# Performance work log

Measured on AMD Instinct MI355X. Metric: run time of the kernel, lower is better.

The kernel has to match this reference:

```python
import jax, jax.numpy as jnp
import numpy as np

N_NODES = 100_000
N_EDGES = 1_600_000
HIDDEN = 32


def setup_inputs() -> dict:
    key = jax.random.key(0)
    ks = jax.random.split(key, 8)
    pos = jax.random.normal(ks[0], (N_NODES, 3), dtype=jnp.float32)
    edge_index = jax.random.randint(ks[1], (2, N_EDGES), 0, N_NODES, dtype=jnp.int64)
    batch = jnp.zeros((N_NODES,), dtype=jnp.int64)
    # layer 1 MLP: Linear(3+3 -> 32) -> ReLU -> Linear(32 -> 32)
    W1 = jax.random.normal(ks[2], (6, HIDDEN), dtype=jnp.float32) * (1.0 / np.sqrt(6))
    b1 = jnp.zeros((HIDDEN,), dtype=jnp.float32)
    W2 = jax.random.normal(ks[3], (HIDDEN, HIDDEN), dtype=jnp.float32) * (1.0 / np.sqrt(HIDDEN))
    b2 = jnp.zeros((HIDDEN,), dtype=jnp.float32)
    # layer 2 MLP: Linear(32+3 -> 32) -> ReLU -> Linear(32 -> 32)
    W3 = jax.random.normal(ks[4], (HIDDEN + 3, HIDDEN), dtype=jnp.float32) * (1.0 / np.sqrt(HIDDEN + 3))
    b3 = jnp.zeros((HIDDEN,), dtype=jnp.float32)
    W4 = jax.random.normal(ks[5], (HIDDEN, HIDDEN), dtype=jnp.float32) * (1.0 / np.sqrt(HIDDEN))
    b4 = jnp.zeros((HIDDEN,), dtype=jnp.float32)
    return {"pos": pos, "edge_index": edge_index, "batch": batch,
            "W1": W1, "b1": b1, "W2": W2, "b2": b2,
            "W3": W3, "b3": b3, "W4": W4, "b4": b4}


def _pointnet_layer(h, rel, src, dst, n_nodes, Wa, ba, Wb, bb):
    # per-edge: concat(h_j, pos_j - pos_i) -> Linear -> ReLU -> Linear, then max-scatter into i
    e = jnp.concatenate([h[src], rel], axis=-1)             # [E, in+3]
    m = jax.nn.relu(e @ Wa + ba) @ Wb + bb                  # [E, out]
    agg = jax.ops.segment_max(m, dst, num_segments=n_nodes)  # [N, out], -inf for isolated nodes
    return jnp.where(jnp.isfinite(agg), agg, 0.0)


def reference(pos, edge_index, batch, W1, b1, W2, b2, W3, b3, W4, b4):
    src = edge_index[0]  # j (source)
    dst = edge_index[1]  # i (target, aggregation index)
    n_nodes = pos.shape[0]
    rel = pos[src] - pos[dst]  # [E, 3]
    h = jax.nn.relu(_pointnet_layer(pos, rel, src, dst, n_nodes, W1, b1, W2, b2))
    h = jax.nn.relu(_pointnet_layer(h, rel, src, dst, n_nodes, W3, b3, W4, b4))
    return h
```

## Files before the change

kernel.cpp:

```cpp
#include <hip/hip_runtime.h>
#include <hip/hip_bf16.h>
#include <stdint.h>


#define BS 256
#define EBS 512
#define K1_EDGES 4096
#define P2_CAP 3072

typedef float v2f __attribute__((ext_vector_type(2)));
typedef __attribute__((ext_vector_type(8))) short bf16x8;
typedef __attribute__((ext_vector_type(16))) float f32x16;
typedef __bf16 bf16v2 __attribute__((ext_vector_type(2)));

__device__ __forceinline__ unsigned ordenc(float f) {
    unsigned u = __float_as_uint(f);
    return (u & 0x80000000u) ? ~u : (u | 0x80000000u);
}
__device__ __forceinline__ float orddec(unsigned o) {
    unsigned u = (o & 0x80000000u) ? (o ^ 0x80000000u) : ~o;
    return __uint_as_float(u);
}
#define ORD_NEG_INF 0x007FFFFFu

__device__ __forceinline__ unsigned cvt2(float x, float y) {
    v2f v = {x, y};
    bf16v2 b = __builtin_convertvector(v, bf16v2);
    return __builtin_bit_cast(unsigned, b);
}
__device__ __forceinline__ float bflo(unsigned u) { return __uint_as_float(u << 16); }
__device__ __forceinline__ float bfhi(unsigned u) { return __uint_as_float(u & 0xFFFF0000u); }

__global__ __launch_bounds__(BS) void setup_kernel(
    const int* __restrict__ ei, int E, int NRP, int* __restrict__ blockHist,
    const float* __restrict__ pos, const float* __restrict__ Wa, const float* __restrict__ ba,
    unsigned* __restrict__ Ubf, float* __restrict__ V, int N, unsigned* __restrict__ aggA,
    unsigned* __restrict__ aggB, int n32, int NB1, int NBn) {
    __shared__ int hist[1024];
    const int tid = threadIdx.x;
    const int b = blockIdx.x;
    if (b < NB1) {
        for (int r = tid; r < 1024; r += BS) hist[r] = 0;
        __syncthreads();
        const int base = b * K1_EDGES;
        const int M = min(K1_EDGES, E - base);
        for (int i = tid; i < M; i += BS) atomicAdd(&hist[ei[E + base + i] >> 7], 1);
        __syncthreads();
        for (int r = tid; r < NRP; r += BS) blockHist[b * NRP + r] = hist[r];
    } else if (b < NB1 + NBn) {
        const int n = (b - NB1) * BS + tid;
        if (n >= N) return;
        const float p[3] = {pos[3 * n], pos[3 * n + 1], pos[3 * n + 2]};
        v2f u[16], v[16];
#pragma unroll
        for (int g = 0; g < 16; ++g) {
            u[g] = *reinterpret_cast<const v2f*>(&ba[g * 2]);
            v2f z = {0.0f, 0.0f};
            v[g] = z;
        }
#pragma unroll
        for (int i = 0; i < 3; ++i) {
            const v2f f = {p[i], p[i]};
#pragma unroll
            for (int g = 0; g < 16; ++g) {
                const v2f wA = *reinterpret_cast<const v2f*>(&Wa[i * 32 + g * 2]);
                const v2f wB = *reinterpret_cast<const v2f*>(&Wa[(i + 3) * 32 + g * 2]);
                u[g] = __builtin_elementwise_fma(f, wA + wB, u[g]);
                v[g] = __builtin_elementwise_fma(f, wB, v[g]);
            }
        }
        uint4* Up = reinterpret_cast<uint4*>(Ubf + (size_t)n * 16);
        float4* Vp = reinterpret_cast<float4*>(V + (size_t)n * 32);
#pragma unroll
        for (int q = 0; q < 4; ++q) {
            uint4 o;
            o.x = cvt2(u[4 * q + 0].x, u[4 * q + 0].y);
            o.y = cvt2(u[4 * q + 1].x, u[4 * q + 1].y);
            o.z = cvt2(u[4 * q + 2].x, u[4 * q + 2].y);
            o.w = cvt2(u[4 * q + 3].x, u[4 * q + 3].y);
            Up[q] = o;
        }
#pragma unroll
        for (int q = 0; q < 8; ++q)
            Vp[q] = make_float4(v[2 * q].x, v[2 * q].y, v[2 * q + 1].x, v[2 * q + 1].y);
    } else {
        const int i = (b - NB1 - NBn) * BS + tid;
        if (i < n32) {
            aggA[i] = ORD_NEG_INF;
            aggB[i] = ORD_NEG_INF;
        }
    }
}

__global__ __launch_bounds__(BS) void finalize_kernel(unsigned* __restrict__ buf, int n) {
    int i = blockIdx.x * BS + threadIdx.x;
    if (i < n) {
        float v = orddec(buf[i]);
        reinterpret_cast<float*>(buf)[i] = fmaxf(v, 0.0f);
    }
}

__global__ __launch_bounds__(512) void off_scan_kernel(const int* __restrict__ blockHist,
                                                       int NB1, int NRP,
                                                       int* __restrict__ off,
                                                       int* __restrict__ total) {
    const int r = (blockIdx.x * 512 + threadIdx.x) >> 6;
    const int lane = threadIdx.x & 63;
    if (r >= NRP) return;
    int carry = 0;
    const int chunks = (NB1 + 63) / 64;
    for (int c = 0; c < chunks; ++c) {
        const int b = c * 64 + lane;
        const int v = (b < NB1) ? blockHist[b * NRP + r] : 0;
        int x = v;
#pragma unroll
        for (int d = 1; d < 64; d <<= 1) {
            int y = __shfl_up(x, d, 64);
            if (lane >= d) x += y;
        }
        if (b < NB1) off[b * NRP + r] = carry + (x - v);
        carry += __shfl(x, 63, 64);
    }
    if (lane == 0) total[r] = carry;
}

__global__ __launch_bounds__(1024) void range_scan_kernel(const int* __restrict__ total,
                                                          int NRP, int* __restrict__ rangeBase) {
    __shared__ int s[1024];
    const int t = threadIdx.x;
    const int v = (t < NRP) ? total[t] : 0;
    s[t] = v;
    __syncthreads();
    for (int off = 1; off < 1024; off <<= 1) {
        int add = (t >= off) ? s[t - off] : 0;
        __syncthreads();
        s[t] += add;
        __syncthreads();
    }
    if (t < NRP) rangeBase[t] = s[t] - v;
}

__global__ __launch_bounds__(BS) void bucket_scatter_kernel(
    const int* __restrict__ ei, int E, int NRP, const int* __restrict__ off,
    const int* __restrict__ rangeBase, int2* __restrict__ sedgeB) {
    __shared__ int2 stage[K1_EDGES];
    __shared__ unsigned short inv[K1_EDGES];
    __shared__ int hist[1024], start[1024], cursor[1024];
    __shared__ int ts[BS];
    const int tid = threadIdx.x;
    for (int r = tid; r < 1024; r += BS) hist[r] = 0;
    __syncthreads();
    const int base = blockIdx.x * K1_EDGES;
    const int M = min(K1_EDGES, E - base);
    for (int i = tid; i < M; i += BS) {
        const int2 p = make_int2(ei[base + i], ei[E + base + i]);
        stage[i] = p;
        atomicAdd(&hist[p.y >> 7], 1);
    }
    __syncthreads();
    {
        const int i0 = tid * 4;
        const int l0 = hist[i0], l1 = hist[i0 + 1], l2 = hist[i0 + 2], l3 = hist[i0 + 3];
        const int tsum = l0 + l1 + l2 + l3;
        ts[tid] = tsum;
        __syncthreads();
        for (int off2 = 1; off2 < BS; off2 <<= 1) {
            int add = (tid >= off2) ? ts[tid - off2] : 0;
            __syncthreads();
            ts[tid] += add;
            __syncthreads();
        }
        const int texcl = ts[tid] - tsum;
        start[i0] = texcl;
        start[i0 + 1] = texcl + l0;
        start[i0 + 2] = texcl + l0 + l1;
        start[i0 + 3] = texcl + l0 + l1 + l2;
        cursor[i0] = start[i0];
        cursor[i0 + 1] = start[i0 + 1];
        cursor[i0 + 2] = start[i0 + 2];
        cursor[i0 + 3] = start[i0 + 3];
    }
    __syncthreads();
    for (int i = tid; i < M; i += BS) {
        const int pos = atomicAdd(&cursor[stage[i].y >> 7], 1);
        inv[pos] = (unsigned short)i;
    }
    __syncthreads();
    const int* offb = off + blockIdx.x * NRP;
    for (int j = tid; j < M; j += BS) {
        const int2 p = stage[inv[j]];
        const int r = p.y >> 7;
        sedgeB[rangeBase[r] + offb[r] + (j - start[r])] = p;
    }
}

__global__ __launch_bounds__(BS) void bucket_sort_kernel(
    const int2* __restrict__ sedgeB, const int* __restrict__ rangeBase,
    const int* __restrict__ total, int N, int2* __restrict__ sedge, int* __restrict__ row_ptr,
    int* __restrict__ cnt) {
    __shared__ int2 stage[P2_CAP];
    __shared__ unsigned short inv[P2_CAP];
    __shared__ int hist[128], start[128], cursor[128];
    const int r = blockIdx.x;
    const int tid = threadIdx.x;
    const int base = rangeBase[r];
    const int M = total[r];
    const bool fast = (M <= P2_CAP);
    if (tid < 128) hist[tid] = 0;
    __syncthreads();
    if (fast) {
        for (int i = tid; i < M; i += BS) {
            const int2 p = sedgeB[base + i];
            stage[i] = p;
            atomicAdd(&hist[p.y & 127], 1);
        }
    } else {
        if (tid < 128) {
            int c = 0;
            for (int i = 0; i < M; ++i) c += ((sedgeB[base + i].y & 127) == tid);
            hist[tid] = c;
        }
    }
    __syncthreads();
    if (tid < 128) start[tid] = hist[tid];
    __syncthreads();
    for (int off2 = 1; off2 < 128; off2 <<= 1) {
        int add = 0;
        if (tid < 128 && tid >= off2) add = start[tid - off2];
        __syncthreads();
        if (tid < 128) start[tid] += add;
        __syncthreads();
    }
    if (tid < 128) {
        const int excl = start[tid] - hist[tid];
        start[tid] = excl;
        cursor[tid] = excl;
        const int node = r * 128 + tid;
        if (node < N) {
            row_ptr[node] = base + excl;
            cnt[node] = hist[tid];
        }
    }
    __syncthreads();
    if (fast) {
        for (int i = tid; i < M; i += BS) {
            const int pos = atomicAdd(&cursor[stage[i].y & 127], 1);
            inv[pos] = (unsigned short)i;
        }
        __syncthreads();
        for (int j = tid; j < M; j += BS) sedge[base + j] = stage[inv[j]];
    } else {
        if (tid < 128) {
            int c = base + start[tid];
            for (int i = 0; i < M; ++i) {
                const int2 p = sedgeB[base + i];
                if ((p.y & 127) == tid) sedge[c++] = p;
            }
        }
    }
}

__global__ __launch_bounds__(BS) void prep2_kernel(const float* __restrict__ pos,
                                                   const unsigned* __restrict__ aggA,
                                                   const float* __restrict__ Wa,
                                                   const float* __restrict__ ba,
                                                   unsigned* __restrict__ Ubf,
                                                   float* __restrict__ V, int N) {
    int n = blockIdx.x * BS + threadIdx.x;
    if (n >= N) return;
    float h[32];
    const uint4* hp = reinterpret_cast<const uint4*>(aggA + (size_t)n * 32);
#pragma unroll
    for (int q = 0; q < 8; ++q) {
        uint4 t = hp[q];
        h[4 * q + 0] = fmaxf(orddec(t.x), 0.0f);
        h[4 * q + 1] = fmaxf(orddec(t.y), 0.0f);
        h[4 * q + 2] = fmaxf(orddec(t.z), 0.0f);
        h[4 * q + 3] = fmaxf(orddec(t.w), 0.0f);
    }
    const float p[3] = {pos[3 * n], pos[3 * n + 1], pos[3 * n + 2]};
    v2f u[16], v[16];
#pragma unroll
    for (int g = 0; g < 16; ++g) {
        u[g] = *reinterpret_cast<const v2f*>(&ba[g * 2]);
        v2f z = {0.0f, 0.0f};
        v[g] = z;
    }
#pragma unroll
    for (int i = 0; i < 32; ++i) {
        const v2f f = {h[i], h[i]};
#pragma unroll
        for (int g = 0; g < 16; ++g) {
            const v2f w = *reinterpret_cast<const v2f*>(&Wa[i * 32 + g * 2]);
            u[g] = __builtin_elementwise_fma(f, w, u[g]);
        }
    }
#pragma unroll
    for (int i = 0; i < 3; ++i) {
        const v2f f = {p[i], p[i]};
#pragma unroll
        for (int g = 0; g < 16; ++g) {
            const v2f w = *reinterpret_cast<const v2f*>(&Wa[(32 + i) * 32 + g * 2]);
            u[g] = __builtin_elementwise_fma(f, w, u[g]);
            v[g] = __builtin_elementwise_fma(f, w, v[g]);
        }
    }
    uint4* Up = reinterpret_cast<uint4*>(Ubf + (size_t)n * 16);
    float4* Vp = reinterpret_cast<float4*>(V + (size_t)n * 32);
#pragma unroll
    for (int q = 0; q < 4; ++q) {
        uint4 o;
        o.x = cvt2(u[4 * q + 0].x, u[4 * q + 0].y);
        o.y = cvt2(u[4 * q + 1].x, u[4 * q + 1].y);
        o.z = cvt2(u[4 * q + 2].x, u[4 * q + 2].y);
        o.w = cvt2(u[4 * q + 3].x, u[4 * q + 3].y);
        Up[q] = o;
    }
#pragma unroll
    for (int q = 0; q < 8; ++q)
        Vp[q] = make_float4(v[2 * q].x, v[2 * q].y, v[2 * q + 1].x, v[2 * q + 1].y);
}

__global__ __launch_bounds__(EBS, 6) void edge_seg_kernel(
    const unsigned* __restrict__ Ubf, const float4* __restrict__ V,
    const int* __restrict__ row_ptr, const int* __restrict__ cnt,
    const int2* __restrict__ sedge, const float* __restrict__ Wb,
    const float* __restrict__ bb, unsigned* __restrict__ agg, int E) {
    __shared__ __align__(16) unsigned lds[10752];

    const int tid = threadIdx.x;
    const int k0 = blockIdx.x * EBS;
    const int blockEnd = min(k0 + EBS, E);
    const int k = min(k0 + tid, E - 1);

    if (tid < 256) {
        const int n = tid & 31;
        const int p = (tid >> 5) * 2;
        lds[10240 + n * 16 + p + 0] = cvt2(Wb[(2 * p + 0) * 32 + n], Wb[(2 * p + 1) * 32 + n]);
        lds[10240 + n * 16 + p + 1] = cvt2(Wb[(2 * p + 2) * 32 + n], Wb[(2 * p + 3) * 32 + n]);
    }

    const int2 ed = sedge[k];
    {
        const uint4* Up = reinterpret_cast<const uint4*>(Ubf + (size_t)ed.x * 16);
        const float4* Vp = V + (size_t)ed.y * 8;
        const uint4 U0 = Up[0];
        const uint4 U1 = Up[1];
        const uint4 U2 = Up[2];
        const uint4 U3 = Up[3];
        const unsigned uu[16] = {U0.x, U0.y, U0.z, U0.w, U1.x, U1.y, U1.z, U1.w,
                                 U2.x, U2.y, U2.z, U2.w, U3.x, U3.y, U3.z, U3.w};
#pragma unroll
        for (int q = 0; q < 8; ++q) {
            const float4 vb = Vp[q];
            const unsigned a = uu[2 * q + 0];
            const unsigned b = uu[2 * q + 1];
            const float h0 = fmaxf(bflo(a) - vb.x, 0.0f);
            const float h1 = fmaxf(bfhi(a) - vb.y, 0.0f);
            const float h2 = fmaxf(bflo(b) - vb.z, 0.0f);
            const float h3 = fmaxf(bfhi(b) - vb.w, 0.0f);
            lds[tid * 20 + 2 * q + 0] = cvt2(h0, h1);
            lds[tid * 20 + 2 * q + 1] = cvt2(h2, h3);
        }
    }
    __syncthreads();

    const int l = tid & 63;
    const int w = tid >> 6;
    const int half = l >> 5;
    const int ln = l & 31;
    const uint4* ldsv = reinterpret_cast<const uint4*>(lds);

    const int e0 = 64 * w + ln;
    const int e1 = e0 + 32;
    const uint4 au00 = ldsv[e0 * 5 + half];
    const uint4 au01 = ldsv[e0 * 5 + half + 2];
    const uint4 au10 = ldsv[e1 * 5 + half];
    const uint4 au11 = ldsv[e1 * 5 + half + 2];
    const uint4 bu0 = ldsv[2560 + ln * 4 + half];
    const uint4 bu1 = ldsv[2560 + ln * 4 + half + 2];
    const float bbn = bb[ln];
    __syncthreads();

    f32x16 c0, c1;
#pragma unroll
    for (int i = 0; i < 16; ++i) {
        c0[i] = bbn;
        c1[i] = bbn;
    }
    c0 = __builtin_amdgcn_mfma_f32_32x32x16_bf16(__builtin_bit_cast(bf16x8, au00),
                                                 __builtin_bit_cast(bf16x8, bu0), c0, 0, 0, 0);
    c0 = __builtin_amdgcn_mfma_f32_32x32x16_bf16(__builtin_bit_cast(bf16x8, au01),
                                                 __builtin_bit_cast(bf16x8, bu1), c0, 0, 0, 0);
    c1 = __builtin_amdgcn_mfma_f32_32x32x16_bf16(__builtin_bit_cast(bf16x8, au10),
                                                 __builtin_bit_cast(bf16x8, bu0), c1, 0, 0, 0);
    c1 = __builtin_amdgcn_mfma_f32_32x32x16_bf16(__builtin_bit_cast(bf16x8, au11),
                                                 __builtin_bit_cast(bf16x8, bu1), c1, 0, 0, 0);

#pragma unroll
    for (int k2 = 0; k2 < 8; ++k2) {
        const int rr = 2 * k2;
        const int er = 64 * w + (rr & 3) + 8 * (rr >> 2) + 4 * half;
        lds[ln * 258 + (er >> 1)] = cvt2(c0[rr], c0[rr + 1]);
        lds[ln * 258 + (er >> 1) + 16] = cvt2(c1[rr], c1[rr + 1]);
    }
    __syncthreads();

    const int d0 = sedge[k0].y;
    const int d1 = sedge[blockEnd - 1].y;
    const int nPairs = (d1 - d0 + 1) * 32;
    for (int idx = tid; idx < nPairs; idx += EBS) {
        const int c = idx & 31;
        const int n = d0 + (idx >> 5);
        const int rs = row_ptr[n];
        const int re = rs + cnt[n];
        const int s0 = max(rs, k0) - k0;
        const int s1 = min(re, blockEnd) - k0;
        if (s0 >= s1) continue;
        const unsigned* smc = &lds[c * 258];
        v2f m0 = {-INFINITY, -INFINITY};
        v2f m1 = m0;
        int e = s0;
        if (e & 1) {
            const unsigned u = smc[e >> 1];
            m0.x = fmaxf(m0.x, bfhi(u));
            ++e;
        }
        for (; e + 4 <= s1; e += 4) {
            const unsigned ua = smc[e >> 1];
            const unsigned ub = smc[(e >> 1) + 1];
            const v2f a = {bflo(ua), bfhi(ua)};
            const v2f b = {bflo(ub), bfhi(ub)};
            m0 = __builtin_elementwise_max(m0, a);
            m1 = __builtin_elementwise_max(m1, b);
        }
        if (e + 2 <= s1) {
            const unsigned u = smc[e >> 1];
            const v2f a = {bflo(u), bfhi(u)};
            m0 = __builtin_elementwise_max(m0, a);
            e += 2;
        }
        if (e < s1) m0.x = fmaxf(m0.x, bflo(smc[e >> 1]));
        const v2f mm = __builtin_elementwise_max(m0, m1);
        const float v = fmaxf(mm.x, mm.y);
        unsigned* p = &agg[(size_t)n * 32 + c];
        const unsigned enc = ordenc(v);
        if (rs >= k0 && re <= blockEnd)
            *p = enc;
        else
            atomicMax(p, enc);
    }
}

extern "C" void kernel_launch(void* const* d_in, const int* in_sizes, int n_in,
                              void* d_out, int out_size, void* d_ws, size_t ws_size,
                              hipStream_t stream) {
    const float* pos = (const float*)d_in[0];
    const int* ei = (const int*)d_in[1];
    const float* W1 = (const float*)d_in[3];
    const float* b1 = (const float*)d_in[4];
    const float* W2 = (const float*)d_in[5];
    const float* b2 = (const float*)d_in[6];
    const float* W3 = (const float*)d_in[7];
    const float* b3 = (const float*)d_in[8];
    const float* W4 = (const float*)d_in[9];
    const float* b4 = (const float*)d_in[10];

    const int E = in_sizes[1] / 2;
    const int N = in_sizes[0] / 3;
    const int n32 = N * 32;
    const int NPAD = ((N + BS - 1) / BS) * BS;
    const int EB2 = (E + EBS - 1) / EBS;
    const int NR = (N + 127) / 128;
    const int NRP = ((NR + 15) / 16) * 16;
    const int NB1 = (E + K1_EDGES - 1) / K1_EDGES;
    const int BH = NB1 * NRP;

    int* cnt = (int*)d_ws;
    int* row_ptr = cnt + NPAD;
    int* blockHist = row_ptr + NPAD;
    int* off = blockHist + BH;
    int* total = off + BH;
    int* rangeBase = total + NRP;
    int2* sedge = (int2*)(rangeBase + NRP);
    int2* sedgeB = sedge + E;
    unsigned* aggA = (unsigned*)(sedgeB + E);
    unsigned* Ubf = aggA + n32;
    float* Vbuf = (float*)(Ubf + (size_t)NPAD * 16);
    unsigned* aggB = (unsigned*)d_out;

    const int gridN32 = (n32 + BS - 1) / BS;
    const int NBn = (N + BS - 1) / BS;

    setup_kernel<<<NB1 + NBn + gridN32, BS, 0, stream>>>(ei, E, NRP, blockHist, pos, W1, b1,
                                                         Ubf, Vbuf, N, aggA, aggB, n32, NB1,
                                                         NBn);
    off_scan_kernel<<<(NRP * 64 + 511) / 512, 512, 0, stream>>>(blockHist, NB1, NRP, off,
                                                                total);
    range_scan_kernel<<<1, 1024, 0, stream>>>(total, NRP, rangeBase);
    bucket_scatter_kernel<<<NB1, BS, 0, stream>>>(ei, E, NRP, off, rangeBase, sedgeB);
    bucket_sort_kernel<<<NR, BS, 0, stream>>>(sedgeB, rangeBase, total, N, sedge, row_ptr, cnt);

    edge_seg_kernel<<<EB2, EBS, 0, stream>>>(Ubf, (const float4*)Vbuf, row_ptr, cnt, sedge, W2,
                                             b2, aggA, E);
    prep2_kernel<<<NBn, BS, 0, stream>>>(pos, aggA, W3, b3, Ubf, Vbuf, N);
    edge_seg_kernel<<<EB2, EBS, 0, stream>>>(Ubf, (const float4*)Vbuf, row_ptr, cnt, sedge, W4,
                                             b4, aggB, E);
    finalize_kernel<<<gridN32, BS, 0, stream>>>(aggB, n32);
}
```

Baseline: 229.9 us.

## Build MFMA A-fragments directly from global loads and pretranspose Wb once

The edge kernel no longer stages per-edge hidden activations through LDS with two barriers. Each lane now gathers exactly the U/V slices its MFMA fragment needs and builds the bf16 operand in registers. The second-layer weight matrices are converted to bf16 fragment layout once, in an extra block of the setup kernel, and read straight from global memory. This removes LDS traffic and barriers and shrinks LDS use, but every edge's gather is now split across two lanes with more scattered loads.

```diff
diff --git a/kernel.cpp b/kernel.cpp
--- a/kernel.cpp
+++ b/kernel.cpp
@@ -31,11 +31,22 @@
 __device__ __forceinline__ float bflo(unsigned u) { return __uint_as_float(u << 16); }
 __device__ __forceinline__ float bfhi(unsigned u) { return __uint_as_float(u & 0xFFFF0000u); }
 
+__device__ __forceinline__ uint4 mk_frag(uint4 ua, float4 v0, float4 v1) {
+    uint4 o;
+    o.x = cvt2(fmaxf(bflo(ua.x) - v0.x, 0.0f), fmaxf(bfhi(ua.x) - v0.y, 0.0f));
+    o.y = cvt2(fmaxf(bflo(ua.y) - v0.z, 0.0f), fmaxf(bfhi(ua.y) - v0.w, 0.0f));
+    o.z = cvt2(fmaxf(bflo(ua.z) - v1.x, 0.0f), fmaxf(bfhi(ua.z) - v1.y, 0.0f));
+    o.w = cvt2(fmaxf(bflo(ua.w) - v1.z, 0.0f), fmaxf(bfhi(ua.w) - v1.w, 0.0f));
+    return o;
+}
+
 __global__ __launch_bounds__(BS) void setup_kernel(
     const int* __restrict__ ei, int E, int NRP, int* __restrict__ blockHist,
     const float* __restrict__ pos, const float* __restrict__ Wa, const float* __restrict__ ba,
     unsigned* __restrict__ Ubf, float* __restrict__ V, int N, unsigned* __restrict__ aggA,
-    unsigned* __restrict__ aggB, int n32, int NB1, int NBn) {
+    unsigned* __restrict__ aggB, int n32, int NB1, int NBn, int gridN32,
+    const float* __restrict__ Wb2, const float* __restrict__ Wb4,
+    unsigned* __restrict__ WbtG) {
     __shared__ int hist[1024];
     const int tid = threadIdx.x;
     const int b = blockIdx.x;
@@ -83,11 +94,26 @@
 #pragma unroll
         for (int q = 0; q < 8; ++q)
             Vp[q] = make_float4(v[2 * q].x, v[2 * q].y, v[2 * q + 1].x, v[2 * q + 1].y);
-    } else {
+    } else if (b < NB1 + NBn + gridN32) {
         const int i = (b - NB1 - NBn) * BS + tid;
         if (i < n32) {
             aggA[i] = ORD_NEG_INF;
             aggB[i] = ORD_NEG_INF;
+        }
+    } else {
+        if (tid < 128) {
+            const int layer = tid >> 6;
+            const int t = tid & 63;
+            const int lnp = t & 31;
+            const int hp = t >> 5;
+            const float* Wb = layer ? Wb4 : Wb2;
+            unsigned* dst = WbtG + layer * 512 + t * 8;
+#pragma unroll
+            for (int q = 0; q < 4; ++q) {
+                const int p = 4 * hp + q;
+                dst[q] = cvt2(Wb[(2 * p) * 32 + lnp], Wb[(2 * p + 1) * 32 + lnp]);
+                dst[4 + q] = cvt2(Wb[(2 * p + 16) * 32 + lnp], Wb[(2 * p + 17) * 32 + lnp]);
+            }
         }
     }
 }
@@ -324,63 +350,45 @@
 __global__ __launch_bounds__(EBS, 6) void edge_seg_kernel(
     const unsigned* __restrict__ Ubf, const float4* __restrict__ V,
     const int* __restrict__ row_ptr, const int* __restrict__ cnt,
-    const int2* __restrict__ sedge, const float* __restrict__ Wb,
+    const int2* __restrict__ sedge, const unsigned* __restrict__ WbtG,
     const float* __restrict__ bb, unsigned* __restrict__ agg, int E) {
-    __shared__ __align__(16) unsigned lds[10752];
+    __shared__ __align__(16) unsigned lds[8256];
 
     const int tid = threadIdx.x;
     const int k0 = blockIdx.x * EBS;
     const int blockEnd = min(k0 + EBS, E);
-    const int k = min(k0 + tid, E - 1);
-
-    if (tid < 256) {
-        const int n = tid & 31;
-        const int p = (tid >> 5) * 2;
-        lds[10240 + n * 16 + p + 0] = cvt2(Wb[(2 * p + 0) * 32 + n], Wb[(2 * p + 1) * 32 + n]);
-        lds[10240 + n * 16 + p + 1] = cvt2(Wb[(2 * p + 2) * 32 + n], Wb[(2 * p + 3) * 32 + n]);
-    }
-
-    const int2 ed = sedge[k];
-    {
-        const uint4* Up = reinterpret_cast<const uint4*>(Ubf + (size_t)ed.x * 16);
-        const float4* Vp = V + (size_t)ed.y * 8;
-        const uint4 U0 = Up[0];
-        const uint4 U1 = Up[1];
-        const uint4 U2 = Up[2];
-        const uint4 U3 = Up[3];
-        const unsigned uu[16] = {U0.x, U0.y, U0.z, U0.w, U1.x, U1.y, U1.z, U1.w,
-                                 U2.x, U2.y, U2.z, U2.w, U3.x, U3.y, U3.z, U3.w};
-#pragma unroll
-        for (int q = 0; q < 8; ++q) {
-            const float4 vb = Vp[q];
-            const unsigned a = uu[2 * q + 0];
-            const unsigned b = uu[2 * q + 1];
-            const float h0 = fmaxf(bflo(a) - vb.x, 0.0f);
-            const float h1 = fmaxf(bfhi(a) - vb.y, 0.0f);
-            const float h2 = fmaxf(bflo(b) - vb.z, 0.0f);
-            const float h3 = fmaxf(bfhi(b) - vb.w, 0.0f);
-            lds[tid * 20 + 2 * q + 0] = cvt2(h0, h1);
-            lds[tid * 20 + 2 * q + 1] = cvt2(h2, h3);
-        }
-    }
-    __syncthreads();
 
     const int l = tid & 63;
     const int w = tid >> 6;
     const int half = l >> 5;
     const int ln = l & 31;
-    const uint4* ldsv = reinterpret_cast<const uint4*>(lds);
-
-    const int e0 = 64 * w + ln;
-    const int e1 = e0 + 32;
-    const uint4 au00 = ldsv[e0 * 5 + half];
-    const uint4 au01 = ldsv[e0 * 5 + half + 2];
-    const uint4 au10 = ldsv[e1 * 5 + half];
-    const uint4 au11 = ldsv[e1 * 5 + half + 2];
-    const uint4 bu0 = ldsv[2560 + ln * 4 + half];
-    const uint4 bu1 = ldsv[2560 + ln * 4 + half + 2];
+
+    const int e0 = min(k0 + 64 * w + ln, E - 1);
+    const int e1 = min(e0 + 32, E - 1);
+
+    const uint4 bu0 = *reinterpret_cast<const uint4*>(WbtG + l * 8);
+    const uint4 bu1 = *reinterpret_cast<const uint4*>(WbtG + l * 8 + 4);
     const float bbn = bb[ln];
-    __syncthreads();
+
+    uint4 au00, au01, au10, au11;
+    {
+        const int2 ed = sedge[e0];
+        const uint4* Up = reinterpret_cast<const uint4*>(Ubf + (size_t)ed.x * 16);
+        const float4* Vp = V + (size_t)ed.y * 8;
+        const uint4 ua = Up[half];
+        const uint4 ub = Up[2 + half];
+        au00 = mk_frag(ua, Vp[2 * half], Vp[2 * half + 1]);
+        au01 = mk_frag(ub, Vp[4 + 2 * half], Vp[5 + 2 * half]);
+    }
+    {
+        const int2 ed = sedge[e1];
+        const uint4* Up = reinterpret_cast<const uint4*>(Ubf + (size_t)ed.x * 16);
+        const float4* Vp = V + (size_t)ed.y * 8;
+        const uint4 ua = Up[half];
+        const uint4 ub = Up[2 + half];
+        au10 = mk_frag(ua, Vp[2 * half], Vp[2 * half + 1]);
+        au11 = mk_frag(ub, Vp[4 + 2 * half], Vp[5 + 2 * half]);
+    }
 
     f32x16 c0, c1;
 #pragma unroll
@@ -487,24 +495,25 @@
     unsigned* aggA = (unsigned*)(sedgeB + E);
     unsigned* Ubf = aggA + n32;
     float* Vbuf = (float*)(Ubf + (size_t)NPAD * 16);
+    unsigned* WbtG = (unsigned*)(Vbuf + n32);
     unsigned* aggB = (unsigned*)d_out;
 
     const int gridN32 = (n32 + BS - 1) / BS;
     const int NBn = (N + BS - 1) / BS;
 
-    setup_kernel<<<NB1 + NBn + gridN32, BS, 0, stream>>>(ei, E, NRP, blockHist, pos, W1, b1,
-                                                         Ubf, Vbuf, N, aggA, aggB, n32, NB1,
-                                                         NBn);
+    setup_kernel<<<NB1 + NBn + gridN32 + 1, BS, 0, stream>>>(
+        ei, E, NRP, blockHist, pos, W1, b1, Ubf, Vbuf, N, aggA, aggB, n32, NB1, NBn,
+        gridN32, W2, W4, WbtG);
     off_scan_kernel<<<(NRP * 64 + 511) / 512, 512, 0, stream>>>(blockHist, NB1, NRP, off,
                                                                 total);
     range_scan_kernel<<<1, 1024, 0, stream>>>(total, NRP, rangeBase);
     bucket_scatter_kernel<<<NB1, BS, 0, stream>>>(ei, E, NRP, off, rangeBase, sedgeB);
     bucket_sort_kernel<<<NR, BS, 0, stream>>>(sedgeB, rangeBase, total, N, sedge, row_ptr, cnt);
 
-    edge_seg_kernel<<<EB2, EBS, 0, stream>>>(Ubf, (const float4*)Vbuf, row_ptr, cnt, sedge, W2,
-                                             b2, aggA, E);
+    edge_seg_kernel<<<EB2, EBS, 0, stream>>>(Ubf, (const float4*)Vbuf, row_ptr, cnt, sedge,
+                                             WbtG, b2, aggA, E);
     prep2_kernel<<<NBn, BS, 0, stream>>>(pos, aggA, W3, b3, Ubf, Vbuf, N);
-    edge_seg_kernel<<<EB2, EBS, 0, stream>>>(Ubf, (const float4*)Vbuf, row_ptr, cnt, sedge, W4,
-                                             b4, aggB, E);
+    edge_seg_kernel<<<EB2, EBS, 0, stream>>>(Ubf, (const float4*)Vbuf, row_ptr, cnt, sedge,
+                                             WbtG + 512, b4, aggB, E);
     finalize_kernel<<<gridN32, BS, 0, stream>>>(aggB, n32);
 }
```

Result: slower. 236.9 us (+3.1%).
